# Optimization experiments

Hardware: AMD Instinct MI355X
Metric: run time of the kernel (lower is better)

Reference implementation:

```python
import jax, jax.numpy as jnp
import numpy as np

D_MODEL = 1024
D_FF = 2048
N_EXPERTS = 8
Z_LOSS_COEF = 0.001


def setup_inputs() -> dict:
    key = jax.random.key(0)
    kx, kr, k1, k3, k2 = jax.random.split(key, 5)
    s_in = 1.0 / np.sqrt(D_MODEL)
    s_ff = 1.0 / np.sqrt(D_FF)
    return {
        "x": jax.random.normal(kx, (4, 2048, D_MODEL), dtype=jnp.float32),
        # router: nn.Linear(d_model, num_experts, bias=False) -> weight [E, D]
        "Wr": jax.random.normal(kr, (N_EXPERTS, D_MODEL), dtype=jnp.float32) * s_in,
        # stacked expert weights, torch Linear layout [out, in]
        "W1": jax.random.normal(k1, (N_EXPERTS, D_FF, D_MODEL), dtype=jnp.float32) * s_in,
        "W3": jax.random.normal(k3, (N_EXPERTS, D_FF, D_MODEL), dtype=jnp.float32) * s_in,
        "W2": jax.random.normal(k2, (N_EXPERTS, D_MODEL, D_FF), dtype=jnp.float32) * s_ff,
    }


def reference(x, Wr, W1, W3, W2):
    B, S, D = x.shape
    E = Wr.shape[0]
    xf = x.reshape(B * S, D)          # [T, D]
    T = xf.shape[0]

    # --- router ---
    logits = xf @ Wr.T                # [T, E]
    probs = jax.nn.softmax(logits, axis=-1)
    top2_p, top2_i = jax.lax.top_k(probs, 2)          # [T, 2]
    top2_p = top2_p / (jnp.sum(top2_p, axis=-1, keepdims=True) + 1e-9)

    # dense gate matrix: zero for unselected experts (same math as index_add combine)
    gates = jnp.zeros((T, E), jnp.float32).at[jnp.arange(T)[:, None], top2_i].add(top2_p)

    # --- experts (SwiGLU), computed per-expert over all tokens, masked by gates ---
    h1 = jax.nn.silu(jnp.einsum('td,efd->etf', xf, W1))   # [E, T, F]
    h3 = jnp.einsum('td,efd->etf', xf, W3)                 # [E, T, F]
    y = jnp.einsum('etf,edf->etd', h1 * h3, W2)            # [E, T, D]
    out = jnp.einsum('etd,te->td', y.astype(jnp.float32), gates)
    out = out.astype(x.dtype).reshape(B, S, D)

    # --- losses ---
    z = jax.nn.logsumexp(logits.astype(jnp.float32), axis=-1)
    router_loss = Z_LOSS_COEF * jnp.mean(z * z)

    importance = jnp.sum(probs.astype(jnp.float32), axis=0) / T   # [E]
    top1 = top2_i[:, 0]
    load = jnp.zeros((E,), jnp.float32).at[top1].add(1.0) / T
    aux_loss = jnp.sum(importance * load) * E

    return out, router_loss, aux_loss
```

## Files before the change

kernel.cpp:

```cpp
#include <hip/hip_runtime.h>
#include <stdint.h>

#define NT 8192
#define DM 1024
#define DF 2048
#define RT_BLOCKS 256

typedef __attribute__((ext_vector_type(8))) short short8;
typedef __attribute__((ext_vector_type(4))) float f32x4;
typedef unsigned short us;

__device__ __forceinline__ us f2bf(float f) {
  uint32_t x = __float_as_uint(f);
  return (us)((x + 0x7fffu + ((x >> 16) & 1u)) >> 16);
}
__device__ __forceinline__ float bf2f(us v) {
  return __uint_as_float(((uint32_t)v) << 16);
}

__device__ __forceinline__ void gload16(const void* g, void* l) {
  __builtin_amdgcn_global_load_lds(
      (const __attribute__((address_space(1))) uint32_t*)g,
      (__attribute__((address_space(3))) uint32_t*)l, 16, 0, 0);
}

__global__ void k_cvtw(const float4* __restrict__ w1, const float4* __restrict__ w3,
                       const float4* __restrict__ w2,
                       short8* __restrict__ w13, short8* __restrict__ w2bf) {
  int s = blockIdx.y;
  const float4* src = (s == 0) ? w1 : (s == 1) ? w3 : w2;
  int n8 = 8 * DF * DM / 8;
  int i = blockIdx.x * blockDim.x + threadIdx.x;
  int st = gridDim.x * blockDim.x;
  for (; i < n8; i += st) {
    float4 va = src[2 * i], vb = src[2 * i + 1];
    short8 o;
    o[0] = (short)f2bf(va.x); o[1] = (short)f2bf(va.y);
    o[2] = (short)f2bf(va.z); o[3] = (short)f2bf(va.w);
    o[4] = (short)f2bf(vb.x); o[5] = (short)f2bf(vb.y);
    o[6] = (short)f2bf(vb.z); o[7] = (short)f2bf(vb.w);
    if (s == 2) {
      w2bf[i] = o;
    } else {
      int e = i >> 18;
      int rem = i & ((1 << 18) - 1);
      int f = rem >> 7;
      int k8 = rem & 127;
      int n = 32 * (f >> 4) + 16 * s + (f & 15);
      w13[((size_t)e << 19) + (size_t)n * 128 + k8] = o;
    }
  }
}

__global__ void k_router(const float* __restrict__ x, const float* __restrict__ wr,
                         int* cntb, int* cnt1, float* imp, float* z2,
                         int* epack, float2* gts, us* __restrict__ xbf) {
  int lane = threadIdx.x & 63;
  int wid = threadIdx.x >> 6;
  const float4* w4 = (const float4*)wr;

  float imp_acc[8] = {0.f, 0.f, 0.f, 0.f, 0.f, 0.f, 0.f, 0.f};
  float z2_acc = 0.f;
  int cb_acc[8] = {0, 0, 0, 0, 0, 0, 0, 0};
  int c1_acc[8] = {0, 0, 0, 0, 0, 0, 0, 0};

  for (int t = blockIdx.x * 4 + wid; t < NT; t += RT_BLOCKS * 4) {
    const float4* x4 = (const float4*)(x + (size_t)t * DM);
    ushort4* xb4 = (ushort4*)(xbf + (size_t)t * DM);
    float4 xv[4];
    #pragma unroll
    for (int j = 0; j < 4; ++j) {
      xv[j] = x4[lane + 64 * j];
      ushort4 o;
      o.x = f2bf(xv[j].x); o.y = f2bf(xv[j].y); o.z = f2bf(xv[j].z); o.w = f2bf(xv[j].w);
      xb4[lane + 64 * j] = o;
    }
    float p[8];
    #pragma unroll
    for (int e = 0; e < 8; ++e) p[e] = 0.f;
    #pragma unroll
    for (int j = 0; j < 4; ++j) {
      #pragma unroll
      for (int e = 0; e < 8; ++e) {
        float4 wv = w4[e * 256 + lane + 64 * j];
        p[e] += xv[j].x * wv.x + xv[j].y * wv.y + xv[j].z * wv.z + xv[j].w * wv.w;
      }
    }
    #pragma unroll
    for (int off = 32; off > 0; off >>= 1) {
      #pragma unroll
      for (int e = 0; e < 8; ++e) p[e] += __shfl_down(p[e], off);
    }
    if (lane == 0) {
      float m = p[0];
      #pragma unroll
      for (int e = 1; e < 8; ++e) m = fmaxf(m, p[e]);
      float pr[8], sum = 0.f;
      #pragma unroll
      for (int e = 0; e < 8; ++e) { pr[e] = expf(p[e] - m); sum += pr[e]; }
      float inv = 1.f / sum;
      #pragma unroll
      for (int e = 0; e < 8; ++e) pr[e] *= inv;
      float z = m + logf(sum);
      int e0 = 0; float b0 = p[0];
      #pragma unroll
      for (int e = 1; e < 8; ++e) { if (p[e] > b0) { b0 = p[e]; e0 = e; } }
      int e1 = -1; float b1 = -1e30f;
      #pragma unroll
      for (int e = 0; e < 8; ++e) { if (e != e0 && p[e] > b1) { b1 = p[e]; e1 = e; } }
      float p0 = 0.f, p1 = 0.f;
      #pragma unroll
      for (int e = 0; e < 8; ++e) {
        p0 = (e == e0) ? pr[e] : p0;
        p1 = (e == e1) ? pr[e] : p1;
      }
      float gs = p0 + p1 + 1e-9f;
      epack[t] = e0 | (e1 << 16);
      gts[t] = make_float2(p0 / gs, p1 / gs);
      z2_acc += z * z;
      #pragma unroll
      for (int e = 0; e < 8; ++e) {
        imp_acc[e] += pr[e];
        cb_acc[e] += (e == e0) + (e == e1);
        c1_acc[e] += (e == e0);
      }
    }
  }

  __shared__ float simp[4][8];
  __shared__ float sz2[4];
  __shared__ int scb[4][8];
  __shared__ int sc1[4][8];
  if (lane == 0) {
    #pragma unroll
    for (int e = 0; e < 8; ++e) { simp[wid][e] = imp_acc[e]; scb[wid][e] = cb_acc[e]; sc1[wid][e] = c1_acc[e]; }
    sz2[wid] = z2_acc;
  }
  __syncthreads();
  int tid = threadIdx.x;
  if (tid < 8) {
    float ss = simp[0][tid] + simp[1][tid] + simp[2][tid] + simp[3][tid];
    int b = scb[0][tid] + scb[1][tid] + scb[2][tid] + scb[3][tid];
    int o = sc1[0][tid] + sc1[1][tid] + sc1[2][tid] + sc1[3][tid];
    atomicAdd(&imp[tid], ss);
    atomicAdd(&cntb[tid], b);
    atomicAdd(&cnt1[tid], o);
  } else if (tid == 8) {
    atomicAdd(z2, sz2[0] + sz2[1] + sz2[2] + sz2[3]);
  }
}

__global__ void k_scatter2(const int* __restrict__ cntb, const int* __restrict__ cnt1,
                           const float* __restrict__ imp, const float* __restrict__ z2,
                           const int* __restrict__ epack,
                           int* __restrict__ offs_g, float* __restrict__ otail,
                           int* __restrict__ btok, int* __restrict__ pos) {
  int e = blockIdx.x;
  int lane = threadIdx.x;
  int offs[8]; int o = 0;
  #pragma unroll
  for (int i = 0; i < 8; ++i) { offs[i] = o; o += cntb[i]; }
  if (e == 0 && lane == 0) {
    #pragma unroll
    for (int i = 0; i < 8; ++i) offs_g[i] = offs[i];
    otail[0] = 1e-3f * z2[0] / (float)NT;
    float aux = 0.f;
    for (int i = 0; i < 8; ++i)
      aux += (imp[i] / (float)NT) * ((float)cnt1[i] / (float)NT);
    otail[1] = aux * 8.f;
  }
  int base = offs[e];
  int run = 0;
  for (int j0 = 0; j0 < 2 * NT; j0 += 64) {
    int j = j0 + lane;
    int t = j >> 1;
    int ep = epack[t];
    int sel = (j & 1) ? (ep >> 16) : (ep & 0xffff);
    bool f = (sel == e);
    unsigned long long m = __ballot(f);
    int rank = __popcll(m & ((1ull << lane) - 1ull));
    if (f) {
      int slot = base + run + rank;
      btok[slot] = t;
      pos[j] = slot;
    }
    run += __popcll(m);
  }
}


__global__ __launch_bounds__(256) void k_ffn1(
    const us* __restrict__ xb, const us* __restrict__ w13,
    const int* __restrict__ offs, const int* __restrict__ cnts,
    const int* __restrict__ btok, us* __restrict__ hg) {
  int e = blockIdx.z;
  int cnt = cnts[e];
  int m0 = blockIdx.y * 128;
  if (m0 >= cnt) return;
  int n0 = blockIdx.x * 128;
  int off = offs[e];
  __shared__ __align__(16) short As[2][4096];
  __shared__ __align__(16) short Bs[2][4096];
  __shared__ int tok[128];
  int tid = threadIdx.x, lane = tid & 63, wid = tid >> 6;
  if (tid < 128) {
    int r = m0 + tid; if (r > cnt - 1) r = cnt - 1;
    tok[tid] = btok[off + r];
  }
  __syncthreads();

  int prow = tid >> 3;
  int pu = (tid & 7) ^ (prow & 7);
  int row0 = prow * 2 + (pu >> 2);
  int gc = (pu & 3) * 8;
  const us* w13e = w13 + ((size_t)e << 22);
  const us* a0 = xb + (size_t)tok[row0] * DM + gc;
  const us* a1 = xb + (size_t)tok[row0 + 64] * DM + gc;
  const us* b0 = w13e + (size_t)(n0 + row0) * DM + gc;
  const us* b1 = w13e + (size_t)(n0 + row0 + 64) * DM + gc;
  int dsl = tid * 8;

  int wm = wid >> 1, wn = wid & 1;
  int fr = lane & 15, glog = lane >> 4;
  int pos = (((fr & 1) << 2) | glog) ^ ((fr >> 1) & 7);
  int aoff = (wm * 32 + (fr >> 1)) * 64 + pos * 8;
  int boff = (wn * 32 + (fr >> 1)) * 64 + pos * 8;
  f32x4 acc[4][4] = {};

  const int NK = DM / 64;
  for (int kt = 0; kt < NK; ++kt) {
    int k0 = kt * 64;
    #pragma unroll
    for (int h = 0; h < 2; ++h) {
      int ko = k0 + h * 32;
      gload16(a0 + ko, &As[h][dsl]);
      gload16(a1 + ko, &As[h][dsl + 2048]);
      gload16(b0 + ko, &Bs[h][dsl]);
      gload16(b1 + ko, &Bs[h][dsl + 2048]);
    }
    __syncthreads();
    #pragma unroll
    for (int h = 0; h < 2; ++h) {
      short8 a[4], b[4];
      #pragma unroll
      for (int mi = 0; mi < 4; ++mi) a[mi] = *(const short8*)&As[h][aoff + mi * 512];
      #pragma unroll
      for (int ni = 0; ni < 4; ++ni) b[ni] = *(const short8*)&Bs[h][boff + ni * 512];
      #pragma unroll
      for (int mi = 0; mi < 4; ++mi) {
        #pragma unroll
        for (int ni = 0; ni < 4; ++ni)
          acc[mi][ni] = __builtin_amdgcn_mfma_f32_16x16x32_bf16(a[mi], b[ni], acc[mi][ni], 0, 0, 0);
      }
    }
    __syncthreads();
  }

  int c = lane & 15, r4 = (lane >> 4) * 4;
  int fb = (n0 + wn * 64) >> 1;
  #pragma unroll
  for (int mi = 0; mi < 4; ++mi) {
    #pragma unroll
    for (int rg = 0; rg < 4; ++rg) {
      int gr = m0 + wm * 64 + mi * 16 + r4 + rg;
      if (gr < cnt) {
        us* hrow = hg + (size_t)(off + gr) * DF;
        #pragma unroll
        for (int j = 0; j < 2; ++j) {
          float a1v = acc[mi][2 * j][rg];
          float a3v = acc[mi][2 * j + 1][rg];
          float h = (a1v / (1.f + __expf(-a1v))) * a3v;
          hrow[fb + j * 16 + c] = f2bf(h);
        }
      }
    }
  }
}

__global__ __launch_bounds__(256) void k_ffn2(
    const us* __restrict__ hg, const us* __restrict__ w2b,
    const int* __restrict__ offs, const int* __restrict__ cnts,
    us* __restrict__ ys) {
  int e = blockIdx.z;
  int cnt = cnts[e];
  int m0 = blockIdx.y * 128;
  if (m0 >= cnt) return;
  int n0 = blockIdx.x * 128;
  int off = offs[e];
  __shared__ __align__(16) short As[2][4096];
  __shared__ __align__(16) short Bs[2][4096];
  int tid = threadIdx.x, lane = tid & 63, wid = tid >> 6;

  int prow = tid >> 3;
  int pu = (tid & 7) ^ (prow & 7);
  int row0 = prow * 2 + (pu >> 2);
  int gc = (pu & 3) * 8;
  int ar0 = m0 + row0;      if (ar0 > cnt - 1) ar0 = cnt - 1;
  int ar1 = m0 + row0 + 64; if (ar1 > cnt - 1) ar1 = cnt - 1;
  const us* w2e = w2b + ((size_t)e << 21);
  const us* a0 = hg + (size_t)(off + ar0) * DF + gc;
  const us* a1 = hg + (size_t)(off + ar1) * DF + gc;
  const us* b0 = w2e + (size_t)(n0 + row0) * DF + gc;
  const us* b1 = w2e + (size_t)(n0 + row0 + 64) * DF + gc;
  int dsl = tid * 8;

  int wm = wid >> 1, wn = wid & 1;
  int fr = lane & 15, glog = lane >> 4;
  int pos = (((fr & 1) << 2) | glog) ^ ((fr >> 1) & 7);
  int aoff = (wm * 32 + (fr >> 1)) * 64 + pos * 8;
  int boff = (wn * 32 + (fr >> 1)) * 64 + pos * 8;
  f32x4 acc[4][4] = {};

  const int NK = DF / 64;
  for (int kt = 0; kt < NK; ++kt) {
    int k0 = kt * 64;
    #pragma unroll
    for (int h = 0; h < 2; ++h) {
      int ko = k0 + h * 32;
      gload16(a0 + ko, &As[h][dsl]);
      gload16(a1 + ko, &As[h][dsl + 2048]);
      gload16(b0 + ko, &Bs[h][dsl]);
      gload16(b1 + ko, &Bs[h][dsl + 2048]);
    }
    __syncthreads();
    #pragma unroll
    for (int h = 0; h < 2; ++h) {
      short8 a[4], b[4];
      #pragma unroll
      for (int mi = 0; mi < 4; ++mi) a[mi] = *(const short8*)&As[h][aoff + mi * 512];
      #pragma unroll
      for (int ni = 0; ni < 4; ++ni) b[ni] = *(const short8*)&Bs[h][boff + ni * 512];
      #pragma unroll
      for (int mi = 0; mi < 4; ++mi) {
        #pragma unroll
        for (int ni = 0; ni < 4; ++ni)
          acc[mi][ni] = __builtin_amdgcn_mfma_f32_16x16x32_bf16(a[mi], b[ni], acc[mi][ni], 0, 0, 0);
      }
    }
    __syncthreads();
  }

  int c = lane & 15, r4 = (lane >> 4) * 4;
  #pragma unroll
  for (int mi = 0; mi < 4; ++mi) {
    #pragma unroll
    for (int rg = 0; rg < 4; ++rg) {
      int gr = m0 + wm * 64 + mi * 16 + r4 + rg;
      if (gr < cnt) {
        us* yrow = ys + (size_t)(off + gr) * DM + n0;
        #pragma unroll
        for (int ni = 0; ni < 4; ++ni)
          yrow[wn * 64 + ni * 16 + c] = f2bf(acc[mi][ni][rg]);
      }
    }
  }
}

__global__ void k_gather(const us* __restrict__ ys, const int* __restrict__ pos,
                         const float2* __restrict__ gts, float* __restrict__ out) {
  int idx = blockIdx.x * blockDim.x + threadIdx.x;
  int t = idx >> 8;
  int d4 = idx & 255;
  float2 g = gts[t];
  ushort4 a = ((const ushort4*)(ys + (size_t)pos[2 * t] * DM))[d4];
  ushort4 b = ((const ushort4*)(ys + (size_t)pos[2 * t + 1] * DM))[d4];
  float4 o;
  o.x = g.x * bf2f(a.x) + g.y * bf2f(b.x);
  o.y = g.x * bf2f(a.y) + g.y * bf2f(b.y);
  o.z = g.x * bf2f(a.z) + g.y * bf2f(b.z);
  o.w = g.x * bf2f(a.w) + g.y * bf2f(b.w);
  ((float4*)out)[idx] = o;
}


extern "C" void kernel_launch(void* const* d_in, const int* in_sizes, int n_in,
                              void* d_out, int out_size, void* d_ws, size_t ws_size,
                              hipStream_t stream) {
  const float* x  = (const float*)d_in[0];
  const float* wr = (const float*)d_in[1];
  const float* w1 = (const float*)d_in[2];
  const float* w3 = (const float*)d_in[3];
  const float* w2 = (const float*)d_in[4];
  float* out = (float*)d_out;

  uint8_t* ws = (uint8_t*)d_ws;
  int*    cntb   = (int*)(ws + 0);
  int*    cnt1   = (int*)(ws + 32);
  int*    offs   = (int*)(ws + 96);
  float*  imp    = (float*)(ws + 128);
  float*  z2     = (float*)(ws + 160);
  int*    epack  = (int*)(ws + 4096);
  float2* gts    = (float2*)(ws + 36864);
  int*    btok   = (int*)(ws + 102400);
  int*    pos    = (int*)(ws + 167936);
  us*     xbf    = (us*)(ws + 233472);
  us*     w13    = (us*)(ws + 17010688);
  us*     w2bf   = (us*)(ws + 84119552);
  us*     hg     = (us*)(ws + 117673984);
  us*     ysb    = (us*)(ws + 17010688);

  hipMemsetAsync(ws, 0, 4096, stream);

  k_router<<<RT_BLOCKS, 256, 0, stream>>>(x, wr, cntb, cnt1, imp, z2, epack, gts, xbf);
  k_cvtw<<<dim3(2048, 3), 256, 0, stream>>>(
      (const float4*)w1, (const float4*)w3, (const float4*)w2,
      (short8*)w13, (short8*)w2bf);

  k_scatter2<<<8, 64, 0, stream>>>(cntb, cnt1, imp, z2, epack,
                                   offs, out + (size_t)NT * DM, btok, pos);

  k_ffn1<<<dim3(32, 128, 8), 256, 0, stream>>>(xbf, w13, offs, cntb, btok, hg);
  k_ffn2<<<dim3(8, 128, 8), 256, 0, stream>>>(hg, w2bf, offs, cntb, ysb);
  k_gather<<<NT * DM / 4 / 256, 256, 0, stream>>>(ysb, pos, gts, out);
}
```

Measured before the change: 516.6 us.

## Widen FFN2 output tile to 256 columns and process two tokens per router wave

```diff
diff --git a/kernel.cpp b/kernel.cpp
--- a/kernel.cpp
+++ b/kernel.cpp
@@ -64,65 +64,80 @@
   int cb_acc[8] = {0, 0, 0, 0, 0, 0, 0, 0};
   int c1_acc[8] = {0, 0, 0, 0, 0, 0, 0, 0};
 
-  for (int t = blockIdx.x * 4 + wid; t < NT; t += RT_BLOCKS * 4) {
-    const float4* x4 = (const float4*)(x + (size_t)t * DM);
-    ushort4* xb4 = (ushort4*)(xbf + (size_t)t * DM);
-    float4 xv[4];
+  for (int t0 = blockIdx.x * 8 + wid * 2; t0 < NT; t0 += RT_BLOCKS * 8) {
+    int t1 = t0 + 1;
+    const float4* xa = (const float4*)(x + (size_t)t0 * DM);
+    const float4* xb = (const float4*)(x + (size_t)t1 * DM);
+    ushort4* ya = (ushort4*)(xbf + (size_t)t0 * DM);
+    ushort4* yb = (ushort4*)(xbf + (size_t)t1 * DM);
+    float4 xv0[4], xv1[4];
     #pragma unroll
     for (int j = 0; j < 4; ++j) {
-      xv[j] = x4[lane + 64 * j];
-      ushort4 o;
-      o.x = f2bf(xv[j].x); o.y = f2bf(xv[j].y); o.z = f2bf(xv[j].z); o.w = f2bf(xv[j].w);
-      xb4[lane + 64 * j] = o;
-    }
-    float p[8];
-    #pragma unroll
-    for (int e = 0; e < 8; ++e) p[e] = 0.f;
+      xv0[j] = xa[lane + 64 * j];
+      xv1[j] = xb[lane + 64 * j];
+      ushort4 o0, o1;
+      o0.x = f2bf(xv0[j].x); o0.y = f2bf(xv0[j].y); o0.z = f2bf(xv0[j].z); o0.w = f2bf(xv0[j].w);
+      o1.x = f2bf(xv1[j].x); o1.y = f2bf(xv1[j].y); o1.z = f2bf(xv1[j].z); o1.w = f2bf(xv1[j].w);
+      ya[lane + 64 * j] = o0;
+      yb[lane + 64 * j] = o1;
+    }
+    float p0[8], p1[8];
+    #pragma unroll
+    for (int e = 0; e < 8; ++e) { p0[e] = 0.f; p1[e] = 0.f; }
     #pragma unroll
     for (int j = 0; j < 4; ++j) {
       #pragma unroll
       for (int e = 0; e < 8; ++e) {
         float4 wv = w4[e * 256 + lane + 64 * j];
-        p[e] += xv[j].x * wv.x + xv[j].y * wv.y + xv[j].z * wv.z + xv[j].w * wv.w;
+        p0[e] += xv0[j].x * wv.x + xv0[j].y * wv.y + xv0[j].z * wv.z + xv0[j].w * wv.w;
+        p1[e] += xv1[j].x * wv.x + xv1[j].y * wv.y + xv1[j].z * wv.z + xv1[j].w * wv.w;
       }
     }
     #pragma unroll
     for (int off = 32; off > 0; off >>= 1) {
       #pragma unroll
-      for (int e = 0; e < 8; ++e) p[e] += __shfl_down(p[e], off);
+      for (int e = 0; e < 8; ++e) {
+        p0[e] += __shfl_down(p0[e], off);
+        p1[e] += __shfl_down(p1[e], off);
+      }
     }
     if (lane == 0) {
-      float m = p[0];
-      #pragma unroll
-      for (int e = 1; e < 8; ++e) m = fmaxf(m, p[e]);
-      float pr[8], sum = 0.f;
-      #pragma unroll
-      for (int e = 0; e < 8; ++e) { pr[e] = expf(p[e] - m); sum += pr[e]; }
-      float inv = 1.f / sum;
-      #pragma unroll
-      for (int e = 0; e < 8; ++e) pr[e] *= inv;
-      float z = m + logf(sum);
-      int e0 = 0; float b0 = p[0];
-      #pragma unroll
-      for (int e = 1; e < 8; ++e) { if (p[e] > b0) { b0 = p[e]; e0 = e; } }
-      int e1 = -1; float b1 = -1e30f;
-      #pragma unroll
-      for (int e = 0; e < 8; ++e) { if (e != e0 && p[e] > b1) { b1 = p[e]; e1 = e; } }
-      float p0 = 0.f, p1 = 0.f;
-      #pragma unroll
-      for (int e = 0; e < 8; ++e) {
-        p0 = (e == e0) ? pr[e] : p0;
-        p1 = (e == e1) ? pr[e] : p1;
-      }
-      float gs = p0 + p1 + 1e-9f;
-      epack[t] = e0 | (e1 << 16);
-      gts[t] = make_float2(p0 / gs, p1 / gs);
-      z2_acc += z * z;
-      #pragma unroll
-      for (int e = 0; e < 8; ++e) {
-        imp_acc[e] += pr[e];
-        cb_acc[e] += (e == e0) + (e == e1);
-        c1_acc[e] += (e == e0);
+      #pragma unroll
+      for (int which = 0; which < 2; ++which) {
+        float* p = which ? p1 : p0;
+        int t = which ? t1 : t0;
+        float m = p[0];
+        #pragma unroll
+        for (int e = 1; e < 8; ++e) m = fmaxf(m, p[e]);
+        float pr[8], sum = 0.f;
+        #pragma unroll
+        for (int e = 0; e < 8; ++e) { pr[e] = expf(p[e] - m); sum += pr[e]; }
+        float inv = 1.f / sum;
+        #pragma unroll
+        for (int e = 0; e < 8; ++e) pr[e] *= inv;
+        float z = m + logf(sum);
+        int e0 = 0; float b0 = p[0];
+        #pragma unroll
+        for (int e = 1; e < 8; ++e) { if (p[e] > b0) { b0 = p[e]; e0 = e; } }
+        int e1 = -1; float b1 = -1e30f;
+        #pragma unroll
+        for (int e = 0; e < 8; ++e) { if (e != e0 && p[e] > b1) { b1 = p[e]; e1 = e; } }
+        float q0 = 0.f, q1 = 0.f;
+        #pragma unroll
+        for (int e = 0; e < 8; ++e) {
+          q0 = (e == e0) ? pr[e] : q0;
+          q1 = (e == e1) ? pr[e] : q1;
+        }
+        float gs = q0 + q1 + 1e-9f;
+        epack[t] = e0 | (e1 << 16);
+        gts[t] = make_float2(q0 / gs, q1 / gs);
+        z2_acc += z * z;
+        #pragma unroll
+        for (int e = 0; e < 8; ++e) {
+          imp_acc[e] += pr[e];
+          cb_acc[e] += (e == e0) + (e == e1);
+          c1_acc[e] += (e == e0);
+        }
       }
     }
   }
@@ -285,10 +300,10 @@
   int cnt = cnts[e];
   int m0 = blockIdx.y * 128;
   if (m0 >= cnt) return;
-  int n0 = blockIdx.x * 128;
+  int n0 = blockIdx.x * 256;
   int off = offs[e];
   __shared__ __align__(16) short As[2][4096];
-  __shared__ __align__(16) short Bs[2][4096];
+  __shared__ __align__(16) short Bs[2][8192];
   int tid = threadIdx.x, lane = tid & 63, wid = tid >> 6;
 
   int prow = tid >> 3;
@@ -302,14 +317,16 @@
   const us* a1 = hg + (size_t)(off + ar1) * DF + gc;
   const us* b0 = w2e + (size_t)(n0 + row0) * DF + gc;
   const us* b1 = w2e + (size_t)(n0 + row0 + 64) * DF + gc;
+  const us* b2 = w2e + (size_t)(n0 + row0 + 128) * DF + gc;
+  const us* b3 = w2e + (size_t)(n0 + row0 + 192) * DF + gc;
   int dsl = tid * 8;
 
   int wm = wid >> 1, wn = wid & 1;
   int fr = lane & 15, glog = lane >> 4;
   int pos = (((fr & 1) << 2) | glog) ^ ((fr >> 1) & 7);
   int aoff = (wm * 32 + (fr >> 1)) * 64 + pos * 8;
-  int boff = (wn * 32 + (fr >> 1)) * 64 + pos * 8;
-  f32x4 acc[4][4] = {};
+  int boff = (wn * 64 + (fr >> 1)) * 64 + pos * 8;
+  f32x4 acc[4][8] = {};
 
   const int NK = DF / 64;
   for (int kt = 0; kt < NK; ++kt) {
@@ -321,20 +338,26 @@
       gload16(a1 + ko, &As[h][dsl + 2048]);
       gload16(b0 + ko, &Bs[h][dsl]);
       gload16(b1 + ko, &Bs[h][dsl + 2048]);
+      gload16(b2 + ko, &Bs[h][dsl + 4096]);
+      gload16(b3 + ko, &Bs[h][dsl + 6144]);
     }
     __syncthreads();
     #pragma unroll
     for (int h = 0; h < 2; ++h) {
-      short8 a[4], b[4];
+      short8 a[4];
       #pragma unroll
       for (int mi = 0; mi < 4; ++mi) a[mi] = *(const short8*)&As[h][aoff + mi * 512];
       #pragma unroll
-      for (int ni = 0; ni < 4; ++ni) b[ni] = *(const short8*)&Bs[h][boff + ni * 512];
-      #pragma unroll
-      for (int mi = 0; mi < 4; ++mi) {
-        #pragma unroll
-        for (int ni = 0; ni < 4; ++ni)
-          acc[mi][ni] = __builtin_amdgcn_mfma_f32_16x16x32_bf16(a[mi], b[ni], acc[mi][ni], 0, 0, 0);
+      for (int nh = 0; nh < 2; ++nh) {
+        short8 b[4];
+        #pragma unroll
+        for (int j = 0; j < 4; ++j) b[j] = *(const short8*)&Bs[h][boff + (nh * 4 + j) * 512];
+        #pragma unroll
+        for (int mi = 0; mi < 4; ++mi) {
+          #pragma unroll
+          for (int j = 0; j < 4; ++j)
+            acc[mi][nh * 4 + j] = __builtin_amdgcn_mfma_f32_16x16x32_bf16(a[mi], b[j], acc[mi][nh * 4 + j], 0, 0, 0);
+        }
       }
     }
     __syncthreads();
@@ -349,8 +372,8 @@
       if (gr < cnt) {
         us* yrow = ys + (size_t)(off + gr) * DM + n0;
         #pragma unroll
-        for (int ni = 0; ni < 4; ++ni)
-          yrow[wn * 64 + ni * 16 + c] = f2bf(acc[mi][ni][rg]);
+        for (int ni = 0; ni < 8; ++ni)
+          yrow[wn * 128 + ni * 16 + c] = f2bf(acc[mi][ni][rg]);
       }
     }
   }
@@ -410,6 +433,6 @@
                                    offs, out + (size_t)NT * DM, btok, pos);
 
   k_ffn1<<<dim3(32, 128, 8), 256, 0, stream>>>(xbf, w13, offs, cntb, btok, hg);
-  k_ffn2<<<dim3(8, 128, 8), 256, 0, stream>>>(hg, w2bf, offs, cntb, ysb);
+  k_ffn2<<<dim3(4, 128, 8), 256, 0, stream>>>(hg, w2bf, offs, cntb, ysb);
   k_gather<<<NT * DM / 4 / 256, 256, 0, stream>>>(ysb, pos, gts, out);
 }
```

Result: slower. 596.8 us (+15.5%).
